# Performance work log

Measured on AMD Instinct MI355X. Metric: run time of the kernel, lower is better.

## Reference

```python
import math
import jax, jax.numpy as jnp
import numpy as np

IN_CH = 256
BIG, SMALL = 15, 3
GHOST_RATIO = 0.23
NK = math.ceil(BIG / SMALL)           # 5
PAD = SMALL // 2                       # 1
MID = BIG // 2                         # 7
REAL_PAD = [MID - i * SMALL - PAD for i in range(NK)]  # [6,3,0,-3,-6]

# Replicate the torch module's deterministic ghost/rep channel split
np.random.seed(123)
_ghostN = int(IN_CH * GHOST_RATIO)     # 58
REPN = IN_CH - _ghostN                 # 198
_ghost = np.sort(np.random.choice(IN_CH, _ghostN, replace=False))
_rep = np.array(sorted(set(range(IN_CH)) - set(_ghost.tolist())), dtype=np.int64)

B, L = 32, 4096
EPS = 1e-5


def _bn(x, g, b):
    # training-mode BatchNorm1d over (B, L) per channel
    m = jnp.mean(x, (0, 2), keepdims=True)
    v = jnp.var(x, (0, 2), keepdims=True)
    return (x - m) * jax.lax.rsqrt(v + EPS) * g[None, :, None] + b[None, :, None]


def _shift(x, p):
    # zero-filled shift along L: out[t] = x[t - p]
    Lx = x.shape[-1]
    if p > 0:
        return jnp.pad(x, ((0, 0), (0, 0), (p, 0)))[..., :Lx]
    if p < 0:
        return jnp.pad(x, ((0, 0), (0, 0), (0, -p)))[..., -Lx:]
    return x


def setup_inputs() -> dict:
    key = jax.random.key(0)
    ks = jax.random.split(key, 3)
    inputs = jax.random.normal(ks[0], (B, IN_CH, L), dtype=jnp.float32)
    lora_w1 = jax.random.normal(ks[1], (REPN * NK, 1, SMALL), dtype=jnp.float32) * 0.1
    lora_w2 = jax.random.normal(ks[2], (REPN * NK, 1, SMALL), dtype=jnp.float32) * 0.1
    ones = jnp.ones((REPN,), jnp.float32)
    zeros = jnp.zeros((REPN,), jnp.float32)
    return {"inputs": inputs, "lora_w1": lora_w1, "lora_w2": lora_w2,
            "gamma1": ones, "beta1": zeros, "gamma2": ones, "beta2": zeros,
            "gamma3": ones, "beta3": zeros}


def reference(inputs, lora_w1, lora_w2, gamma1, beta1, gamma2, beta2, gamma3, beta3):
    rep_in = inputs[:, _rep, :]        # [B, repN, L]
    ghost_in = inputs[:, _ghost, :]    # [B, ghostN, L]
    # sum of N_path depthwise convs == one conv with summed weights
    w = lora_w1 + lora_w2              # [repN*nk, 1, small]
    out = jax.lax.conv_general_dilated(
        rep_in, w, window_strides=(1,), padding=[(PAD, PAD)],
        dimension_numbers=("NCH", "OIH", "NCH"), feature_group_count=REPN)
    b, _, l = out.shape
    o = out.reshape(b, REPN, NK, l)    # torch grouped conv: group-major channel order
    # shift-add decomposition: reconstruct big-kernel responses from nk small-conv slices
    x1 = sum(_shift(o[:, :, i, :], REAL_PAD[i]) for i in range(NK))
    x2 = sum(_shift(o[:, :, i, :], -REAL_PAD[i]) for i in range(NK))
    x3 = o[:, :, NK // 2, :]           # zero-shift (small-kernel) slice
    x1 = _bn(x1, gamma1, beta1)
    x2 = _bn(x2, gamma2, beta2)
    x3 = _bn(x3, gamma3, beta3)
    x = x1 + x2 + x3 + rep_in
    return jnp.concatenate([x, ghost_in], axis=1)  # [B, C, L]
```

## Files before the change

kernel.cpp:

```cpp
#include <hip/hip_runtime.h>
#include <hip/hip_bf16.h>

#define LEN 4096
#define BATCH 32
#define CH 256
#define REPN 198
#define GHOSTN 58
#define NROW (REPN * BATCH)
#define NGHOST (GHOSTN * BATCH)
#define CPT 16

typedef float f32x4 __attribute__((ext_vector_type(4)));

struct MTState { unsigned mt[624]; int mti; };
struct Tab { int rep[REPN]; int ghost[GHOSTN]; };

static constexpr unsigned mt_next(MTState& s) {
    if (s.mti >= 624) {
        for (int k = 0; k < 624; ++k) {
            unsigned y = (s.mt[k] & 0x80000000u) | (s.mt[(k + 1) % 624] & 0x7fffffffu);
            s.mt[k] = s.mt[(k + 397) % 624] ^ (y >> 1) ^ ((y & 1u) ? 0x9908b0dfu : 0u);
        }
        s.mti = 0;
    }
    unsigned y = s.mt[s.mti++];
    y ^= y >> 11;
    y ^= (y << 7) & 0x9d2c5680u;
    y ^= (y << 15) & 0xefc60000u;
    y ^= y >> 18;
    return y;
}

static constexpr Tab make_tab() {
    MTState s{};
    s.mt[0] = 123u;
    for (int i = 1; i < 624; ++i)
        s.mt[i] = 1812433253u * (s.mt[i - 1] ^ (s.mt[i - 1] >> 30)) + (unsigned)i;
    s.mti = 624;
    int perm[256] = {};
    for (int i = 0; i < 256; ++i) perm[i] = i;
    for (int i = 255; i > 0; --i) {
        unsigned mask = (unsigned)i;
        mask |= mask >> 1; mask |= mask >> 2; mask |= mask >> 4;
        mask |= mask >> 8; mask |= mask >> 16;
        unsigned j = 0;
        do { j = mt_next(s) & mask; } while (j > (unsigned)i);
        int t = perm[i]; perm[i] = perm[j]; perm[j] = t;
    }
    bool g[256] = {};
    for (int k = 0; k < GHOSTN; ++k) g[perm[k]] = true;
    Tab t{};
    int rc = 0, gc = 0;
    for (int c = 0; c < 256; ++c) {
        if (g[c]) t.ghost[gc++] = c;
        else      t.rep[rc++] = c;
    }
    return t;
}

__constant__ Tab d_tab = make_tab();

__global__ __launch_bounds__(256) void pass1_kernel(const float* __restrict__ x,
                                                    const float* __restrict__ w1,
                                                    const float* __restrict__ w2,
                                                    float* __restrict__ stats_ws,
                                                    float* __restrict__ out) {
    const int blk = blockIdx.x;
    if (blk >= NROW) {
        const int g = (blk - NROW) % GHOSTN;
        const int b = (blk - NROW) / GHOSTN;
        const int ch = d_tab.ghost[g];
        const f32x4* src = (const f32x4*)(x + ((size_t)b * CH + ch) * LEN);
        f32x4* dst = (f32x4*)(out + ((size_t)b * CH + REPN + g) * LEN);
#pragma unroll
        for (int k = 0; k < 4; ++k) {
            f32x4 t = __builtin_nontemporal_load(&src[threadIdx.x + 256 * k]);
            __builtin_nontemporal_store(t, &dst[threadIdx.x + 256 * k]);
        }
        return;
    }
    __shared__ float s[LEN + 16];
    __shared__ float red[6][4];
    const int r = blk % REPN;
    const int b = blk / REPN;
    const int ch = d_tab.rep[r];
    const float* row = x + ((size_t)b * CH + ch) * LEN;

    {
        const f32x4* row4 = (const f32x4*)row;
        f32x4* s4 = (f32x4*)(s + 8);
#pragma unroll
        for (int k = 0; k < 4; ++k) s4[threadIdx.x + 256 * k] = row4[threadIdx.x + 256 * k];
        if (threadIdx.x < 8) { s[threadIdx.x] = 0.f; s[LEN + 8 + threadIdx.x] = 0.f; }
    }

    float w[5][3];
    const float* p1 = w1 + r * 15;
    const float* p2 = w2 + r * 15;
#pragma unroll
    for (int i = 0; i < 5; ++i)
#pragma unroll
        for (int t = 0; t < 3; ++t) w[i][t] = p1[i * 3 + t] + p2[i * 3 + t];
    __syncthreads();

    const int l0 = threadIdx.x * CPT;
    float v[32];
    {
        const f32x4* sw = (const f32x4*)(s + l0);
#pragma unroll
        for (int k = 0; k < 8; ++k) {
            f32x4 t = sw[k];
            v[4 * k] = t.x; v[4 * k + 1] = t.y; v[4 * k + 2] = t.z; v[4 * k + 3] = t.w;
        }
    }

    float s1 = 0, s1q = 0, s2 = 0, s2q = 0, s3 = 0, s3q = 0;
    const bool edge = (threadIdx.x == 0) | (threadIdx.x == 255);
#define STAT_BODY(GATED)                                                          \
    _Pragma("unroll")                                                             \
    for (int j = 0; j < CPT; ++j) {                                               \
        const int l = l0 + j;                                                     \
        float x1 = 0.f, x2 = 0.f, x3 = 0.f;                                       \
        _Pragma("unroll")                                                         \
        for (int i = 0; i < 5; ++i) {                                             \
            float a1 = fmaf(w[i][0], v[j + 1 + 3 * i],                            \
                       fmaf(w[i][1], v[j + 2 + 3 * i],                            \
                            w[i][2] * v[j + 3 + 3 * i]));                         \
            float a2 = fmaf(w[i][0], v[j + 13 - 3 * i],                           \
                       fmaf(w[i][1], v[j + 14 - 3 * i],                           \
                            w[i][2] * v[j + 15 - 3 * i]));                        \
            if (i == 2) x3 = a1;                                     \
            if (GATED) {                                                          \
                a1 = ((unsigned)(l - 6 + 3 * i) < (unsigned)LEN) ? a1 : 0.f;      \
                a2 = ((unsigned)(l + 6 - 3 * i) < (unsigned)LEN) ? a2 : 0.f;      \
            }                                                                     \
            x1 += a1; x2 += a2;                                                   \
        }                                                                         \
        s1 += x1; s1q = fmaf(x1, x1, s1q);                                        \
        s2 += x2; s2q = fmaf(x2, x2, s2q);                                        \
        s3 += x3; s3q = fmaf(x3, x3, s3q);                                        \
    }
    if (!edge) { STAT_BODY(false) } else { STAT_BODY(true) }
#undef STAT_BODY

#pragma unroll
    for (int off = 32; off > 0; off >>= 1) {
        s1 += __shfl_down(s1, off);  s1q += __shfl_down(s1q, off);
        s2 += __shfl_down(s2, off);  s2q += __shfl_down(s2q, off);
        s3 += __shfl_down(s3, off);  s3q += __shfl_down(s3q, off);
    }
    const int lane = threadIdx.x & 63, wv = threadIdx.x >> 6;
    if (lane == 0) {
        red[0][wv] = s1; red[1][wv] = s1q;
        red[2][wv] = s2; red[3][wv] = s2q;
        red[4][wv] = s3; red[5][wv] = s3q;
    }
    __syncthreads();
    if (threadIdx.x < 6) {
        float t = red[threadIdx.x][0] + red[threadIdx.x][1] +
                  red[threadIdx.x][2] + red[threadIdx.x][3];
        stats_ws[(threadIdx.x * REPN + r) * BATCH + b] = t;
    }
}

__device__ __forceinline__ void load_fast(const float* __restrict__ row, int e, float* v) {
    const f32x4* q4 = (const f32x4*)(row + e - 8);
#pragma unroll
    for (int t = 0; t < 5; ++t) {
        f32x4 u = q4[t];
        v[4 * t] = u.x; v[4 * t + 1] = u.y; v[4 * t + 2] = u.z; v[4 * t + 3] = u.w;
    }
}

__device__ __forceinline__ void load_slow(const float* __restrict__ row, int e, float* v) {
#pragma unroll
    for (int d = 0; d < 20; ++d) {
        int fi = e - 8 + d;
        v[d] = ((unsigned)fi < (unsigned)LEN) ? row[fi] : 0.f;
    }
}

__global__ __launch_bounds__(256) void pass2_kernel(const float* __restrict__ x,
                                                    const float* __restrict__ w1,
                                                    const float* __restrict__ w2,
                                                    const float* __restrict__ stats_ws,
                                                    const float* __restrict__ g1, const float* __restrict__ b1,
                                                    const float* __restrict__ g2, const float* __restrict__ b2,
                                                    const float* __restrict__ g3, const float* __restrict__ b3,
                                                    float* __restrict__ out) {
    const int wv = (blockIdx.x << 2) | (threadIdx.x >> 6);
    const int lane = threadIdx.x & 63;
    const int r = wv % REPN;
    const int b = wv / REPN;
    const int ch = d_tab.rep[r];
    const float* row = x + ((size_t)b * CH + ch) * LEN;

    float p[6];
    const int bb = lane & 31;
#pragma unroll
    for (int q = 0; q < 6; ++q) p[q] = stats_ws[(q * REPN + r) * BATCH + bb];
#pragma unroll
    for (int m = 1; m < 32; m <<= 1)
#pragma unroll
        for (int q = 0; q < 6; ++q) p[q] += __shfl_xor(p[q], m);

    const double invN = 1.0 / (double)(BATCH * LEN);
    float sc[3], sh[3];
    {
        const float gr[3] = {g1[r], g2[r], g3[r]};
        const float br[3] = {b1[r], b2[r], b3[r]};
#pragma unroll
        for (int q = 0; q < 3; ++q) {
            double mean = (double)p[2 * q] * invN;
            double var = (double)p[2 * q + 1] * invN - mean * mean;
            double inv = 1.0 / sqrt(var + 1e-5);
            double scale = (double)gr[q] * inv;
            sc[q] = (float)scale;
            sh[q] = (float)((double)br[q] - mean * scale);
        }
    }
    const float base = sh[0] + sh[1] + sh[2];

    float wb[5][3];
    const float* p1 = w1 + r * 15;
    const float* p2 = w2 + r * 15;
#pragma unroll
    for (int i = 0; i < 5; ++i)
#pragma unroll
        for (int t = 0; t < 3; ++t) wb[i][t] = p1[i * 3 + t] + p2[i * 3 + t];

    float c[15];
#pragma unroll
    for (int k = 0; k < 5; ++k)
#pragma unroll
        for (int t = 0; t < 3; ++t)
            c[3 * k + t] = fmaf(sc[0], wb[k][t], sc[1] * wb[4 - k][t]);
#pragma unroll
    for (int t = 0; t < 3; ++t) c[6 + t] = fmaf(sc[2], wb[2][t], c[6 + t]);

    float* orow = out + ((size_t)b * CH + r) * LEN;
    float v[20];

#define INTERIOR_QUAD(E)                                                          \
    {                                                                             \
        float o[4];                                                               \
        _Pragma("unroll")                                                         \
        for (int j = 0; j < 4; ++j) {                                             \
            float acc = base + v[j + 8];                                          \
            _Pragma("unroll")                                                     \
            for (int d = 0; d < 15; ++d) acc = fmaf(c[d], v[j + 1 + d], acc);     \
            o[j] = acc;                                                           \
        }                                                                         \
        f32x4 t = {o[0], o[1], o[2], o[3]};                                       \
        __builtin_nontemporal_store(t, (f32x4*)(orow + (E)));                     \
    }

#define EDGE_QUAD(E)                                                              \
    {                                                                             \
        float o[4];                                                               \
        _Pragma("unroll")                                                         \
        for (int j = 0; j < 4; ++j) {                                             \
            const int l = (E) + j;                                                \
            float x1 = 0.f, x2 = 0.f, x3 = 0.f;                                   \
            _Pragma("unroll")                                                     \
            for (int i = 0; i < 5; ++i) {                                         \
                float a1 = fmaf(wb[i][0], v[j + 1 + 3 * i],                       \
                           fmaf(wb[i][1], v[j + 2 + 3 * i],                       \
                                wb[i][2] * v[j + 3 + 3 * i]));                    \
                float a2 = fmaf(wb[i][0], v[j + 13 - 3 * i],                      \
                           fmaf(wb[i][1], v[j + 14 - 3 * i],                      \
                                wb[i][2] * v[j + 15 - 3 * i]));                   \
                if (i == 2) x3 = a1;                                              \
                a1 = ((unsigned)(l - 6 + 3 * i) < (unsigned)LEN) ? a1 : 0.f;      \
                a2 = ((unsigned)(l + 6 - 3 * i) < (unsigned)LEN) ? a2 : 0.f;      \
                x1 += a1; x2 += a2;                                               \
            }                                                                     \
            o[j] = fmaf(sc[0], x1, fmaf(sc[1], x2, fmaf(sc[2], x3, base + v[j + 8]))); \
        }                                                                         \
        f32x4 t = {o[0], o[1], o[2], o[3]};                                       \
        __builtin_nontemporal_store(t, (f32x4*)(orow + (E)));                     \
    }

    {
        const int e = 4 * lane;
        if (lane < 2) { load_slow(row, e, v); EDGE_QUAD(e); }
        else          { load_fast(row, e, v); INTERIOR_QUAD(e); }
    }
#pragma unroll
    for (int k = 1; k < 15; ++k) {
        const int e = 4 * lane + 256 * k;
        load_fast(row, e, v);
        INTERIOR_QUAD(e);
    }
    {
        const int e = 4 * lane + 3840;
        if (lane >= 62) { load_slow(row, e, v); EDGE_QUAD(e); }
        else            { load_fast(row, e, v); INTERIOR_QUAD(e); }
    }
#undef INTERIOR_QUAD
#undef EDGE_QUAD
}

extern "C" void kernel_launch(void* const* d_in, const int* in_sizes, int n_in,
                              void* d_out, int out_size, void* d_ws, size_t ws_size,
                              hipStream_t stream) {
    const float* x  = (const float*)d_in[0];
    const float* w1 = (const float*)d_in[1];
    const float* w2 = (const float*)d_in[2];
    const float* g1 = (const float*)d_in[3];
    const float* b1 = (const float*)d_in[4];
    const float* g2 = (const float*)d_in[5];
    const float* b2 = (const float*)d_in[6];
    const float* g3 = (const float*)d_in[7];
    const float* b3 = (const float*)d_in[8];
    float* out = (float*)d_out;
    float* stats_ws = (float*)d_ws;

    pass1_kernel<<<NROW + NGHOST, 256, 0, stream>>>(x, w1, w2, stats_ws, out);
    pass2_kernel<<<1584, 256, 0, stream>>>(x, w1, w2, stats_ws,
                                           g1, b1, g2, b2, g3, b3, out);
}
```

Baseline: 95.72 us.

## Fuse stats and normalize passes into one per-channel kernel

Replaces the two-kernel scheme with a single kernel that assigns one 1024-thread block per channel. Each wave handles two batch rows, block-wide reduction of the batch-norm statistics happens in shared memory, and the same block then writes the normalized output. This removes the global stats workspace, the second launch and the cross-kernel dependency. In exchange the grid shrinks to 256 blocks with in-block serialization of the two phases, and the ghost copy moves into per-channel blocks looping over batch, which may reduce parallelism and latency hiding.

```diff
diff --git a/kernel.cpp b/kernel.cpp
--- a/kernel.cpp
+++ b/kernel.cpp
@@ -1,14 +1,10 @@
 #include <hip/hip_runtime.h>
-#include <hip/hip_bf16.h>
 
 #define LEN 4096
 #define BATCH 32
 #define CH 256
 #define REPN 198
 #define GHOSTN 58
-#define NROW (REPN * BATCH)
-#define NGHOST (GHOSTN * BATCH)
-#define CPT 16
 
 typedef float f32x4 __attribute__((ext_vector_type(4)));
 
@@ -60,88 +56,114 @@
 
 __constant__ Tab d_tab = make_tab();
 
-__global__ __launch_bounds__(256) void pass1_kernel(const float* __restrict__ x,
-                                                    const float* __restrict__ w1,
-                                                    const float* __restrict__ w2,
-                                                    float* __restrict__ stats_ws,
-                                                    float* __restrict__ out) {
+__device__ __forceinline__ void load_fast(const float* __restrict__ row, int e, float* v) {
+    const f32x4* q4 = (const f32x4*)(row + e - 8);
+#pragma unroll
+    for (int t = 0; t < 5; ++t) {
+        f32x4 u = q4[t];
+        v[4 * t] = u.x; v[4 * t + 1] = u.y; v[4 * t + 2] = u.z; v[4 * t + 3] = u.w;
+    }
+}
+
+__device__ __forceinline__ void load_slow(const float* __restrict__ row, int e, float* v) {
+#pragma unroll
+    for (int d = 0; d < 20; ++d) {
+        int fi = e - 8 + d;
+        v[d] = ((unsigned)fi < (unsigned)LEN) ? row[fi] : 0.f;
+    }
+}
+
+__global__ __launch_bounds__(1024, 4) void mono_kernel(
+    const float* __restrict__ x,
+    const float* __restrict__ w1, const float* __restrict__ w2,
+    const float* __restrict__ g1, const float* __restrict__ b1,
+    const float* __restrict__ g2, const float* __restrict__ b2,
+    const float* __restrict__ g3, const float* __restrict__ b3,
+    float* __restrict__ out) {
     const int blk = blockIdx.x;
-    if (blk >= NROW) {
-        const int g = (blk - NROW) % GHOSTN;
-        const int b = (blk - NROW) / GHOSTN;
-        const int ch = d_tab.ghost[g];
-        const f32x4* src = (const f32x4*)(x + ((size_t)b * CH + ch) * LEN);
-        f32x4* dst = (f32x4*)(out + ((size_t)b * CH + REPN + g) * LEN);
-#pragma unroll
-        for (int k = 0; k < 4; ++k) {
-            f32x4 t = __builtin_nontemporal_load(&src[threadIdx.x + 256 * k]);
-            __builtin_nontemporal_store(t, &dst[threadIdx.x + 256 * k]);
+    const int tid = threadIdx.x;
+
+    if (blk >= REPN) {
+        const int gi = blk - REPN;
+        const int ch = d_tab.ghost[gi];
+#pragma unroll 1
+        for (int b = 0; b < BATCH; ++b) {
+            const f32x4* src = (const f32x4*)(x + ((size_t)b * CH + ch) * LEN);
+            f32x4* dst = (f32x4*)(out + ((size_t)b * CH + REPN + gi) * LEN);
+            f32x4 t = __builtin_nontemporal_load(&src[tid]);
+            __builtin_nontemporal_store(t, &dst[tid]);
         }
         return;
     }
-    __shared__ float s[LEN + 16];
-    __shared__ float red[6][4];
-    const int r = blk % REPN;
-    const int b = blk / REPN;
+
+    __shared__ float red[6][16];
+    const int r = blk;
     const int ch = d_tab.rep[r];
-    const float* row = x + ((size_t)b * CH + ch) * LEN;
-
+    const int wv = tid >> 6;
+    const int lane = tid & 63;
+
+    float wb[5][3];
     {
-        const f32x4* row4 = (const f32x4*)row;
-        f32x4* s4 = (f32x4*)(s + 8);
-#pragma unroll
-        for (int k = 0; k < 4; ++k) s4[threadIdx.x + 256 * k] = row4[threadIdx.x + 256 * k];
-        if (threadIdx.x < 8) { s[threadIdx.x] = 0.f; s[LEN + 8 + threadIdx.x] = 0.f; }
-    }
-
-    float w[5][3];
-    const float* p1 = w1 + r * 15;
-    const float* p2 = w2 + r * 15;
-#pragma unroll
-    for (int i = 0; i < 5; ++i)
-#pragma unroll
-        for (int t = 0; t < 3; ++t) w[i][t] = p1[i * 3 + t] + p2[i * 3 + t];
-    __syncthreads();
-
-    const int l0 = threadIdx.x * CPT;
-    float v[32];
-    {
-        const f32x4* sw = (const f32x4*)(s + l0);
-#pragma unroll
-        for (int k = 0; k < 8; ++k) {
-            f32x4 t = sw[k];
-            v[4 * k] = t.x; v[4 * k + 1] = t.y; v[4 * k + 2] = t.z; v[4 * k + 3] = t.w;
-        }
+        const float* p1 = w1 + r * 15;
+        const float* p2 = w2 + r * 15;
+#pragma unroll
+        for (int i = 0; i < 5; ++i)
+#pragma unroll
+            for (int t = 0; t < 3; ++t) wb[i][t] = p1[i * 3 + t] + p2[i * 3 + t];
     }
 
     float s1 = 0, s1q = 0, s2 = 0, s2q = 0, s3 = 0, s3q = 0;
-    const bool edge = (threadIdx.x == 0) | (threadIdx.x == 255);
-#define STAT_BODY(GATED)                                                          \
-    _Pragma("unroll")                                                             \
-    for (int j = 0; j < CPT; ++j) {                                               \
-        const int l = l0 + j;                                                     \
-        float x1 = 0.f, x2 = 0.f, x3 = 0.f;                                       \
+    float v[20];
+
+#define STATQ(E, GATED)                                                           \
+    {                                                                             \
         _Pragma("unroll")                                                         \
-        for (int i = 0; i < 5; ++i) {                                             \
-            float a1 = fmaf(w[i][0], v[j + 1 + 3 * i],                            \
-                       fmaf(w[i][1], v[j + 2 + 3 * i],                            \
-                            w[i][2] * v[j + 3 + 3 * i]));                         \
-            float a2 = fmaf(w[i][0], v[j + 13 - 3 * i],                           \
-                       fmaf(w[i][1], v[j + 14 - 3 * i],                           \
-                            w[i][2] * v[j + 15 - 3 * i]));                        \
-            if (i == 2) x3 = a1;                                     \
-            if (GATED) {                                                          \
-                a1 = ((unsigned)(l - 6 + 3 * i) < (unsigned)LEN) ? a1 : 0.f;      \
-                a2 = ((unsigned)(l + 6 - 3 * i) < (unsigned)LEN) ? a2 : 0.f;      \
+        for (int j = 0; j < 4; ++j) {                                             \
+            const int l = (E) + j;                                                \
+            float x1 = 0.f, x2 = 0.f, x3 = 0.f;                                   \
+            _Pragma("unroll")                                                     \
+            for (int i = 0; i < 5; ++i) {                                         \
+                float a1 = fmaf(wb[i][0], v[j + 1 + 3 * i],                       \
+                           fmaf(wb[i][1], v[j + 2 + 3 * i],                       \
+                                wb[i][2] * v[j + 3 + 3 * i]));                    \
+                float a2 = fmaf(wb[i][0], v[j + 13 - 3 * i],                      \
+                           fmaf(wb[i][1], v[j + 14 - 3 * i],                      \
+                                wb[i][2] * v[j + 15 - 3 * i]));                   \
+                if (i == 2) x3 = a1;                                 \
+                if (GATED) {                                                      \
+                    a1 = ((unsigned)(l - 6 + 3 * i) < (unsigned)LEN) ? a1 : 0.f;  \
+                    a2 = ((unsigned)(l + 6 - 3 * i) < (unsigned)LEN) ? a2 : 0.f;  \
+                }                                                                 \
+                x1 += a1; x2 += a2;                                               \
             }                                                                     \
-            x1 += a1; x2 += a2;                                                   \
+            s1 += x1; s1q = fmaf(x1, x1, s1q);                                    \
+            s2 += x2; s2q = fmaf(x2, x2, s2q);                                    \
+            s3 += x3; s3q = fmaf(x3, x3, s3q);                                    \
         }                                                                         \
-        s1 += x1; s1q = fmaf(x1, x1, s1q);                                        \
-        s2 += x2; s2q = fmaf(x2, x2, s2q);                                        \
-        s3 += x3; s3q = fmaf(x3, x3, s3q);                                        \
-    }
-    if (!edge) { STAT_BODY(false) } else { STAT_BODY(true) }
-#undef STAT_BODY
+    }
+
+#pragma unroll 1
+    for (int bb = 0; bb < 2; ++bb) {
+        const int b = 2 * wv + bb;
+        const float* row = x + ((size_t)b * CH + ch) * LEN;
+        {
+            const int e = 4 * lane;
+            if (lane < 2) { load_slow(row, e, v); STATQ(e, true); }
+            else          { load_fast(row, e, v); STATQ(e, false); }
+        }
+#pragma unroll 2
+        for (int k = 1; k < 15; ++k) {
+            const int e = 4 * lane + 256 * k;
+            load_fast(row, e, v);
+            STATQ(e, false);
+        }
+        {
+            const int e = 4 * lane + 3840;
+            if (lane >= 62) { load_slow(row, e, v); STATQ(e, true); }
+            else            { load_fast(row, e, v); STATQ(e, false); }
+        }
+    }
+#undef STATQ
 
 #pragma unroll
     for (int off = 32; off > 0; off >>= 1) {
@@ -149,61 +171,21 @@
         s2 += __shfl_down(s2, off);  s2q += __shfl_down(s2q, off);
         s3 += __shfl_down(s3, off);  s3q += __shfl_down(s3q, off);
     }
-    const int lane = threadIdx.x & 63, wv = threadIdx.x >> 6;
     if (lane == 0) {
         red[0][wv] = s1; red[1][wv] = s1q;
         red[2][wv] = s2; red[3][wv] = s2q;
         red[4][wv] = s3; red[5][wv] = s3q;
     }
     __syncthreads();
-    if (threadIdx.x < 6) {
-        float t = red[threadIdx.x][0] + red[threadIdx.x][1] +
-                  red[threadIdx.x][2] + red[threadIdx.x][3];
-        stats_ws[(threadIdx.x * REPN + r) * BATCH + b] = t;
-    }
-}
-
-__device__ __forceinline__ void load_fast(const float* __restrict__ row, int e, float* v) {
-    const f32x4* q4 = (const f32x4*)(row + e - 8);
-#pragma unroll
-    for (int t = 0; t < 5; ++t) {
-        f32x4 u = q4[t];
-        v[4 * t] = u.x; v[4 * t + 1] = u.y; v[4 * t + 2] = u.z; v[4 * t + 3] = u.w;
-    }
-}
-
-__device__ __forceinline__ void load_slow(const float* __restrict__ row, int e, float* v) {
-#pragma unroll
-    for (int d = 0; d < 20; ++d) {
-        int fi = e - 8 + d;
-        v[d] = ((unsigned)fi < (unsigned)LEN) ? row[fi] : 0.f;
-    }
-}
-
-__global__ __launch_bounds__(256) void pass2_kernel(const float* __restrict__ x,
-                                                    const float* __restrict__ w1,
-                                                    const float* __restrict__ w2,
-                                                    const float* __restrict__ stats_ws,
-                                                    const float* __restrict__ g1, const float* __restrict__ b1,
-                                                    const float* __restrict__ g2, const float* __restrict__ b2,
-                                                    const float* __restrict__ g3, const float* __restrict__ b3,
-                                                    float* __restrict__ out) {
-    const int wv = (blockIdx.x << 2) | (threadIdx.x >> 6);
-    const int lane = threadIdx.x & 63;
-    const int r = wv % REPN;
-    const int b = wv / REPN;
-    const int ch = d_tab.rep[r];
-    const float* row = x + ((size_t)b * CH + ch) * LEN;
 
     float p[6];
-    const int bb = lane & 31;
-#pragma unroll
-    for (int q = 0; q < 6; ++q) p[q] = stats_ws[(q * REPN + r) * BATCH + bb];
-#pragma unroll
-    for (int m = 1; m < 32; m <<= 1)
-#pragma unroll
-        for (int q = 0; q < 6; ++q) p[q] += __shfl_xor(p[q], m);
-
+#pragma unroll
+    for (int q = 0; q < 6; ++q) {
+        float t = 0.f;
+#pragma unroll
+        for (int wvi = 0; wvi < 16; ++wvi) t += red[q][wvi];
+        p[q] = t;
+    }
     const double invN = 1.0 / (double)(BATCH * LEN);
     float sc[3], sh[3];
     {
@@ -221,14 +203,6 @@
     }
     const float base = sh[0] + sh[1] + sh[2];
 
-    float wb[5][3];
-    const float* p1 = w1 + r * 15;
-    const float* p2 = w2 + r * 15;
-#pragma unroll
-    for (int i = 0; i < 5; ++i)
-#pragma unroll
-        for (int t = 0; t < 3; ++t) wb[i][t] = p1[i * 3 + t] + p2[i * 3 + t];
-
     float c[15];
 #pragma unroll
     for (int k = 0; k < 5; ++k)
@@ -237,9 +211,6 @@
             c[3 * k + t] = fmaf(sc[0], wb[k][t], sc[1] * wb[4 - k][t]);
 #pragma unroll
     for (int t = 0; t < 3; ++t) c[6 + t] = fmaf(sc[2], wb[2][t], c[6 + t]);
-
-    float* orow = out + ((size_t)b * CH + r) * LEN;
-    float v[20];
 
 #define INTERIOR_QUAD(E)                                                          \
     {                                                                             \
@@ -281,21 +252,27 @@
         __builtin_nontemporal_store(t, (f32x4*)(orow + (E)));                     \
     }
 
-    {
-        const int e = 4 * lane;
-        if (lane < 2) { load_slow(row, e, v); EDGE_QUAD(e); }
-        else          { load_fast(row, e, v); INTERIOR_QUAD(e); }
-    }
-#pragma unroll
-    for (int k = 1; k < 15; ++k) {
-        const int e = 4 * lane + 256 * k;
-        load_fast(row, e, v);
-        INTERIOR_QUAD(e);
-    }
-    {
-        const int e = 4 * lane + 3840;
-        if (lane >= 62) { load_slow(row, e, v); EDGE_QUAD(e); }
-        else            { load_fast(row, e, v); INTERIOR_QUAD(e); }
+#pragma unroll 1
+    for (int bb = 0; bb < 2; ++bb) {
+        const int b = 2 * wv + bb;
+        const float* row = x + ((size_t)b * CH + ch) * LEN;
+        float* orow = out + ((size_t)b * CH + r) * LEN;
+        {
+            const int e = 4 * lane;
+            if (lane < 2) { load_slow(row, e, v); EDGE_QUAD(e); }
+            else          { load_fast(row, e, v); INTERIOR_QUAD(e); }
+        }
+#pragma unroll
+        for (int k = 1; k < 15; ++k) {
+            const int e = 4 * lane + 256 * k;
+            load_fast(row, e, v);
+            INTERIOR_QUAD(e);
+        }
+        {
+            const int e = 4 * lane + 3840;
+            if (lane >= 62) { load_slow(row, e, v); EDGE_QUAD(e); }
+            else            { load_fast(row, e, v); INTERIOR_QUAD(e); }
+        }
     }
 #undef INTERIOR_QUAD
 #undef EDGE_QUAD
@@ -314,9 +291,7 @@
     const float* g3 = (const float*)d_in[7];
     const float* b3 = (const float*)d_in[8];
     float* out = (float*)d_out;
-    float* stats_ws = (float*)d_ws;
-
-    pass1_kernel<<<NROW + NGHOST, 256, 0, stream>>>(x, w1, w2, stats_ws, out);
-    pass2_kernel<<<1584, 256, 0, stream>>>(x, w1, w2, stats_ws,
-                                           g1, b1, g2, b2, g3, b3, out);
-}
+
+    mono_kernel<<<REPN + GHOSTN, 1024, 0, stream>>>(x, w1, w2,
+                                                    g1, b1, g2, b2, g3, b3, out);
+}
```

Measured after the change: 213.0 us. 2.23x slower.
